# Kernel tuning notes

Hardware: AMD Instinct MI355X
Metric: run time of the kernel (lower is better)

The kernel has to match this reference:

```python
import jax, jax.numpy as jnp
import numpy as np

# Involution-style aggregation (SAN Aggregation, pad_mode=0 / zero padding)
K, STRIDE, PAD, DIL = 3, 1, 1, 1


def setup_inputs() -> dict:
    key = jax.random.key(0)
    k1, k2 = jax.random.split(key)
    B, C, H, W = 8, 256, 64, 64
    WC = 16  # weight channels (channel groups share a kernel)
    OH = (H + 2 * PAD - (DIL * (K - 1) + 1)) // STRIDE + 1
    OW = (W + 2 * PAD - (DIL * (K - 1) + 1)) // STRIDE + 1
    x = jax.random.normal(k1, (B, C, H, W), dtype=jnp.float32)
    weight = jax.random.normal(k2, (B, WC, K * K, OH * OW), dtype=jnp.float32)
    return {"x": x, "weight": weight}


def reference(x, weight):
    B, C, H, W = x.shape
    _, WC, K2, _ = weight.shape
    OH = (H + 2 * PAD - (DIL * (K - 1) + 1)) // STRIDE + 1
    OW = (W + 2 * PAD - (DIL * (K - 1) + 1)) // STRIDE + 1
    G = C // WC  # channel groups sharing each dynamic kernel
    xp = jnp.pad(x, ((0, 0), (0, 0), (PAD, PAD), (PAD, PAD)))  # zero pad
    # weight per tap: [B, 1, WC, OH, OW] broadcast over groups
    w = weight.reshape(B, 1, WC, K2, OH, OW)
    out = jnp.zeros((B, G, WC, OH, OW), dtype=x.dtype)
    # fixed small K^2 loop over kernel taps; accumulate without materializing
    # the full unfolded [B, C, K^2, OH, OW] tensor
    for idx in range(K2):
        i, j = idx // K, idx % K
        xs = xp[:, :, i * DIL:i * DIL + (OH - 1) * STRIDE + 1:STRIDE,
                      j * DIL:j * DIL + (OW - 1) * STRIDE + 1:STRIDE]
        out = out + xs.reshape(B, G, WC, OH, OW) * w[:, :, :, idx]
    return out.reshape(B, C, OH, OW)
```

## Files before the change

kernel.cpp:

```cpp
#include <hip/hip_runtime.h>


#define NB 8
#define NC 256
#define NH 64
#define NW 64
#define NWC 16
#define NG 16
#define STRIP 16
#define LCHR 18
#define LROW 64
#define LCH (LCHR * LROW)

typedef float f32x4 __attribute__((ext_vector_type(4)));

__device__ __forceinline__ float dpp_shr1(float v) {
    return __int_as_float(__builtin_amdgcn_update_dpp(
        0, __float_as_int(v), 0x111, 0xf, 0xf, true));
}
__device__ __forceinline__ float dpp_shl1(float v) {
    return __int_as_float(__builtin_amdgcn_update_dpp(
        0, __float_as_int(v), 0x101, 0xf, 0xf, true));
}

__global__ __launch_bounds__(256, 2) void agg_kernel(const float* __restrict__ x,
                                                     const float* __restrict__ wt,
                                                     float* __restrict__ out) {
    __shared__ float lds[NG * LCH];

    const int tid = threadIdx.x;
    const int l16 = tid & 15;
    const int row = tid >> 4;

    const int hw   = blockIdx.x;
    const int bid  = (hw & 7) * 64 + (hw >> 3);
    const int q    = bid & 3;
    const int wc   = (bid >> 2) & 15;
    const int b    = bid >> 6;

    const int oh  = q * STRIP + row;
    const int ow0 = l16 * 4;
    const int r0  = q * STRIP - 1;

    float4 sv[18];
    int    laddr[18];
#pragma unroll
    for (int k = 0; k < 18; ++k) {
        const int f   = tid + k * 256;
        const int ch  = f / 288;
        const int rem = f - ch * 288;
        const int r   = rem >> 4;
        const int c4  = rem & 15;
        const int gr  = r0 + r;
        float4 v = make_float4(0.f, 0.f, 0.f, 0.f);
        if ((unsigned)gr < (unsigned)NH) {
            const int c = ch * NWC + wc;
            v = *reinterpret_cast<const float4*>(
                x + (((b * NC + c) * NH + gr) * NW) + c4 * 4);
        }
        sv[k]    = v;
        laddr[k] = ch * LCH + r * LROW + c4 * 4;
    }

    float w[9][4];
    {
        const float* wp = wt + ((b * NWC + wc) * 9) * (NH * NW) + oh * NW + ow0;
#pragma unroll
        for (int idx = 0; idx < 9; ++idx) {
            float4 t = *reinterpret_cast<const float4*>(wp + idx * (NH * NW));
            w[idx][0] = t.x; w[idx][1] = t.y; w[idx][2] = t.z; w[idx][3] = t.w;
        }
    }

#pragma unroll
    for (int k = 0; k < 18; ++k) {
        *reinterpret_cast<float4*>(&lds[laddr[k]]) = sv[k];
    }

    __syncthreads();

#pragma unroll
    for (int ch = 0; ch < NG; ++ch) {
        const float* pch = &lds[ch * LCH];
        float acc[4] = {0.f, 0.f, 0.f, 0.f};

#pragma unroll
        for (int i = 0; i < 3; ++i) {
            const float* p = pch + (row + i) * LROW + ow0;
            float4 m = *reinterpret_cast<const float4*>(p);
            const float e0 = dpp_shr1(m.w);
            const float e5 = dpp_shl1(m.x);
            const float e[6] = {e0, m.x, m.y, m.z, m.w, e5};
#pragma unroll
            for (int j = 0; j < 3; ++j) {
                const float* wj = w[i * 3 + j];
                acc[0] += e[0 + j] * wj[0];
                acc[1] += e[1 + j] * wj[1];
                acc[2] += e[2 + j] * wj[2];
                acc[3] += e[3 + j] * wj[3];
            }
        }

        float* op = out + (((b * NC + ch * NWC + wc) * NH + oh) * NW) + ow0;
        f32x4 o = {acc[0], acc[1], acc[2], acc[3]};
        __builtin_nontemporal_store(o, reinterpret_cast<f32x4*>(op));
    }
}

extern "C" void kernel_launch(void* const* d_in, const int* in_sizes, int n_in,
                              void* d_out, int out_size, void* d_ws, size_t ws_size,
                              hipStream_t stream) {
    const float* x  = (const float*)d_in[0];
    const float* wt = (const float*)d_in[1];
    float* out      = (float*)d_out;

    dim3 grid(NB * NWC * 4);
    dim3 block(256);
    agg_kernel<<<grid, block, 0, stream>>>(x, wt, out);
}
```

Measured before the change: 20.83 us.

## Drop LDS staging, read halo rows from global and split channel groups across blocks

Removes the shared-memory tile and its barrier. Each thread now loads its three input rows (above, centre, below) straight from global memory, relying on L1/L2 to absorb the halo reuse between neighbouring rows. The group loop is split in two, so the grid doubles and each block does 8 groups instead of 16; launch bounds are raised to 4 blocks per CU. The cost is that the weight taps are loaded twice and global/cache traffic for x rises about threefold; the gain is no LDS write/read round trip and better latency hiding from higher occupancy.

```diff
diff --git a/kernel.cpp b/kernel.cpp
--- a/kernel.cpp
+++ b/kernel.cpp
@@ -7,10 +7,8 @@
 #define NW 64
 #define NWC 16
 #define NG 16
-#define STRIP 16
-#define LCHR 18
-#define LROW 64
-#define LCH (LCHR * LROW)
+#define GPB 8
+#define GSPLIT 2
 
 typedef float f32x4 __attribute__((ext_vector_type(4)));
 
@@ -23,44 +21,22 @@
         0, __float_as_int(v), 0x101, 0xf, 0xf, true));
 }
 
-__global__ __launch_bounds__(256, 2) void agg_kernel(const float* __restrict__ x,
+__global__ __launch_bounds__(256, 4) void agg_kernel(const float* __restrict__ x,
                                                      const float* __restrict__ wt,
                                                      float* __restrict__ out) {
-    __shared__ float lds[NG * LCH];
-
     const int tid = threadIdx.x;
     const int l16 = tid & 15;
     const int row = tid >> 4;
 
     const int hw   = blockIdx.x;
-    const int bid  = (hw & 7) * 64 + (hw >> 3);
+    const int bid  = (hw & 7) * 128 + (hw >> 3);
     const int q    = bid & 3;
-    const int wc   = (bid >> 2) & 15;
-    const int b    = bid >> 6;
+    const int gblk = (bid >> 2) & 1;
+    const int wc   = (bid >> 3) & 15;
+    const int b    = bid >> 7;
 
-    const int oh  = q * STRIP + row;
+    const int oh  = q * 16 + row;
     const int ow0 = l16 * 4;
-    const int r0  = q * STRIP - 1;
-
-    float4 sv[18];
-    int    laddr[18];
-#pragma unroll
-    for (int k = 0; k < 18; ++k) {
-        const int f   = tid + k * 256;
-        const int ch  = f / 288;
-        const int rem = f - ch * 288;
-        const int r   = rem >> 4;
-        const int c4  = rem & 15;
-        const int gr  = r0 + r;
-        float4 v = make_float4(0.f, 0.f, 0.f, 0.f);
-        if ((unsigned)gr < (unsigned)NH) {
-            const int c = ch * NWC + wc;
-            v = *reinterpret_cast<const float4*>(
-                x + (((b * NC + c) * NH + gr) * NW) + c4 * 4);
-        }
-        sv[k]    = v;
-        laddr[k] = ch * LCH + r * LROW + c4 * 4;
-    }
 
     float w[9][4];
     {
@@ -72,22 +48,24 @@
         }
     }
 
-#pragma unroll
-    for (int k = 0; k < 18; ++k) {
-        *reinterpret_cast<float4*>(&lds[laddr[k]]) = sv[k];
-    }
-
-    __syncthreads();
+    const bool has_up   = (oh > 0);
+    const bool has_down = (oh < NH - 1);
 
 #pragma unroll
-    for (int ch = 0; ch < NG; ++ch) {
-        const float* pch = &lds[ch * LCH];
+    for (int cc = 0; cc < GPB; ++cc) {
+        const int c = (gblk * GPB + cc) * NWC + wc;
+        const float* xc = x + ((b * NC + c) * NH) * NW + ow0;
+
+        const float4 z = make_float4(0.f, 0.f, 0.f, 0.f);
+        float4 r[3];
+        r[0] = has_up   ? *reinterpret_cast<const float4*>(xc + (oh - 1) * NW) : z;
+        r[1] =            *reinterpret_cast<const float4*>(xc + oh * NW);
+        r[2] = has_down ? *reinterpret_cast<const float4*>(xc + (oh + 1) * NW) : z;
+
         float acc[4] = {0.f, 0.f, 0.f, 0.f};
-
 #pragma unroll
         for (int i = 0; i < 3; ++i) {
-            const float* p = pch + (row + i) * LROW + ow0;
-            float4 m = *reinterpret_cast<const float4*>(p);
+            const float4 m = r[i];
             const float e0 = dpp_shr1(m.w);
             const float e5 = dpp_shl1(m.x);
             const float e[6] = {e0, m.x, m.y, m.z, m.w, e5};
@@ -101,7 +79,7 @@
             }
         }
 
-        float* op = out + (((b * NC + ch * NWC + wc) * NH + oh) * NW) + ow0;
+        float* op = out + (((b * NC + c) * NH + oh) * NW) + ow0;
         f32x4 o = {acc[0], acc[1], acc[2], acc[3]};
         __builtin_nontemporal_store(o, reinterpret_cast<f32x4*>(op));
     }
@@ -114,7 +92,7 @@
     const float* wt = (const float*)d_in[1];
     float* out      = (float*)d_out;
 
-    dim3 grid(NB * NWC * 4);
+    dim3 grid(NB * NWC * GSPLIT * 4);
     dim3 block(256);
     agg_kernel<<<grid, block, 0, stream>>>(x, wt, out);
 }
```

Measured after the change: 25.60 us. 22.9% more time.

## Stage input via direct global-to-LDS loads in two overlapped channel halves

Applied to the files above, without the earlier changes.

Replaces the register-staged float4 loads and LDS stores with global_load_lds direct-to-LDS transfers. The LDS tile is split into two halves of 8 channels each, so the second half's load is issued before the first half is computed. Out-of-range halo rows read from a zeroed device buffer instead of using a predicated register zero. The aim is to cut VGPR staging and instruction overhead and to overlap load latency with FMA work, at the cost of an extra barrier and reliance on the barrier's implicit vmcnt wait.

```diff
diff --git a/kernel.cpp b/kernel.cpp
--- a/kernel.cpp
+++ b/kernel.cpp
@@ -10,9 +10,12 @@
 #define STRIP 16
 #define LCHR 18
 #define LROW 64
-#define LCH (LCHR * LROW)
+#define LCHF (LCHR * LROW)
+#define HALF_FLOATS (8 * LCHF)
 
 typedef float f32x4 __attribute__((ext_vector_type(4)));
+
+__device__ float g_zero16[16];
 
 __device__ __forceinline__ float dpp_shr1(float v) {
     return __int_as_float(__builtin_amdgcn_update_dpp(
@@ -23,44 +26,50 @@
         0, __float_as_int(v), 0x101, 0xf, 0xf, true));
 }
 
+__device__ __forceinline__ void gld_lds16(const float* src, float* ldsDst) {
+    __builtin_amdgcn_global_load_lds(
+        (const __attribute__((address_space(1))) void*)src,
+        (__attribute__((address_space(3))) void*)ldsDst, 16, 0, 0);
+}
+
 __global__ __launch_bounds__(256, 2) void agg_kernel(const float* __restrict__ x,
                                                      const float* __restrict__ wt,
                                                      float* __restrict__ out) {
-    __shared__ float lds[NG * LCH];
+    __shared__ float lds[2 * HALF_FLOATS];
 
     const int tid = threadIdx.x;
     const int l16 = tid & 15;
     const int row = tid >> 4;
 
-    const int hw   = blockIdx.x;
-    const int bid  = (hw & 7) * 64 + (hw >> 3);
-    const int q    = bid & 3;
-    const int wc   = (bid >> 2) & 15;
-    const int b    = bid >> 6;
+    const int hw  = blockIdx.x;
+    const int bid = (hw & 7) * 64 + (hw >> 3);
+    const int q   = bid & 3;
+    const int wc  = (bid >> 2) & 15;
+    const int b   = bid >> 6;
 
     const int oh  = q * STRIP + row;
     const int ow0 = l16 * 4;
     const int r0  = q * STRIP - 1;
+    const int wavebase = tid & 192;
 
-    float4 sv[18];
-    int    laddr[18];
+    auto stage_half = [&](int h) {
 #pragma unroll
-    for (int k = 0; k < 18; ++k) {
-        const int f   = tid + k * 256;
-        const int ch  = f / 288;
-        const int rem = f - ch * 288;
-        const int r   = rem >> 4;
-        const int c4  = rem & 15;
-        const int gr  = r0 + r;
-        float4 v = make_float4(0.f, 0.f, 0.f, 0.f);
-        if ((unsigned)gr < (unsigned)NH) {
-            const int c = ch * NWC + wc;
-            v = *reinterpret_cast<const float4*>(
-                x + (((b * NC + c) * NH + gr) * NW) + c4 * 4);
+        for (int k = 0; k < 9; ++k) {
+            const int f   = tid + k * 256;
+            const int ch  = f / 288;
+            const int rem = f - ch * 288;
+            const int r   = rem >> 4;
+            const int c4  = rem & 15;
+            const int gr  = r0 + r;
+            const int c   = (h * 8 + ch) * NWC + wc;
+            const float* src = ((unsigned)gr < (unsigned)NH)
+                ? x + (((b * NC + c) * NH + gr) * NW) + c4 * 4
+                : g_zero16;
+            gld_lds16(src, &lds[h * HALF_FLOATS + (wavebase + k * 256) * 4]);
         }
-        sv[k]    = v;
-        laddr[k] = ch * LCH + r * LROW + c4 * 4;
-    }
+    };
+
+    stage_half(0);
 
     float w[9][4];
     {
@@ -72,39 +81,43 @@
         }
     }
 
+    auto compute_half = [&](int h) {
 #pragma unroll
-    for (int k = 0; k < 18; ++k) {
-        *reinterpret_cast<float4*>(&lds[laddr[k]]) = sv[k];
-    }
+        for (int ch = 0; ch < 8; ++ch) {
+            const float* pch = &lds[h * HALF_FLOATS + ch * LCHF];
+            float acc[4] = {0.f, 0.f, 0.f, 0.f};
+#pragma unroll
+            for (int i = 0; i < 3; ++i) {
+                const float* p = pch + (row + i) * LROW + ow0;
+                float4 m = *reinterpret_cast<const float4*>(p);
+                const float e0 = dpp_shr1(m.w);
+                const float e5 = dpp_shl1(m.x);
+                const float e[6] = {e0, m.x, m.y, m.z, m.w, e5};
+#pragma unroll
+                for (int j = 0; j < 3; ++j) {
+                    const float* wj = w[i * 3 + j];
+                    acc[0] += e[0 + j] * wj[0];
+                    acc[1] += e[1 + j] * wj[1];
+                    acc[2] += e[2 + j] * wj[2];
+                    acc[3] += e[3 + j] * wj[3];
+                }
+            }
+            const int c = (h * 8 + ch) * NWC + wc;
+            float* op = out + (((b * NC + c) * NH + oh) * NW) + ow0;
+            f32x4 o = {acc[0], acc[1], acc[2], acc[3]};
+            __builtin_nontemporal_store(o, reinterpret_cast<f32x4*>(op));
+        }
+    };
 
     __syncthreads();
 
-#pragma unroll
-    for (int ch = 0; ch < NG; ++ch) {
-        const float* pch = &lds[ch * LCH];
-        float acc[4] = {0.f, 0.f, 0.f, 0.f};
+    stage_half(1);
 
-#pragma unroll
-        for (int i = 0; i < 3; ++i) {
-            const float* p = pch + (row + i) * LROW + ow0;
-            float4 m = *reinterpret_cast<const float4*>(p);
-            const float e0 = dpp_shr1(m.w);
-            const float e5 = dpp_shl1(m.x);
-            const float e[6] = {e0, m.x, m.y, m.z, m.w, e5};
-#pragma unroll
-            for (int j = 0; j < 3; ++j) {
-                const float* wj = w[i * 3 + j];
-                acc[0] += e[0 + j] * wj[0];
-                acc[1] += e[1 + j] * wj[1];
-                acc[2] += e[2 + j] * wj[2];
-                acc[3] += e[3 + j] * wj[3];
-            }
-        }
+    compute_half(0);
 
-        float* op = out + (((b * NC + ch * NWC + wc) * NH + oh) * NW) + ow0;
-        f32x4 o = {acc[0], acc[1], acc[2], acc[3]};
-        __builtin_nontemporal_store(o, reinterpret_cast<f32x4*>(op));
-    }
+    __syncthreads();
+
+    compute_half(1);
 }
 
 extern "C" void kernel_launch(void* const* d_in, const int* in_sizes, int n_in,
```

After: 20.94 us. About the same (+0.5%).
